# Performance work log

Measured on AMD Instinct MI355X. Metric: run time of the kernel, lower is better.

## Reference

```python
import jax, jax.numpy as jnp
import numpy as np
import math

B, L, D, H = 2, 2048, 1024, 16

def setup_inputs() -> dict:
    key = jax.random.key(0)
    ks = jax.random.split(key, 5)
    return {
        "query": jax.random.normal(ks[0], (B, L, D), dtype=jnp.float32),
        "key": jax.random.normal(ks[1], (B, L, D), dtype=jnp.float32),
        "value": jax.random.normal(ks[2], (B, L, D), dtype=jnp.float32),
        "w_out": jax.random.normal(ks[3], (D, D), dtype=jnp.float32) * (1.0 / math.sqrt(D)),
        "b_out": jnp.zeros((D,), dtype=jnp.float32),
    }

def reference(query, key, value, w_out, b_out):
    b, l, d_model = query.shape
    num_heads = H
    head_dim = d_model // num_heads
    scaling = 1.0 / math.sqrt(d_model)  # NOTE: module scales by embed_dim, not head_dim

    def reshape(x):
        return x.reshape(b, l, num_heads, head_dim).transpose(0, 2, 1, 3)  # [B,H,L,hd]

    q, k, v = reshape(query), reshape(key), reshape(value)
    scores = jnp.einsum("bhqd,bhkd->bhqk", q, k) * scaling  # [B,H,L,L]

    u = max(1, int(math.ceil(math.log(l + 1))))  # static: 8 for L=2048
    _, topk_idx = jax.lax.top_k(scores, u)  # [B,H,L,u]

    # scatter True at top-u key positions per query
    bi = jnp.arange(b)[:, None, None, None]
    hi = jnp.arange(num_heads)[None, :, None, None]
    qi = jnp.arange(l)[None, None, :, None]
    mask = jnp.zeros(scores.shape, dtype=bool).at[bi, hi, qi, topk_idx].set(True)

    scores_masked = jnp.where(mask, scores, -jnp.inf)
    attn_weights = jax.nn.softmax(scores_masked, axis=-1)  # [B,H,L,L]

    attn_out = jnp.einsum("bhqk,bhkd->bhqd", attn_weights, v)
    attn_out = attn_out.transpose(0, 2, 1, 3).reshape(b, l, d_model)
    attn_out = attn_out @ w_out.T + b_out  # nn.Linear
    return attn_out, attn_weights
```

## Files before the change

### kernel.cpp

```cpp
#include <hip/hip_runtime.h>
#include <math.h>

#define BB 2
#define LL 2048
#define DD 1024
#define HH 16
#define SCALE 0.03125f

#define ATTN_ELEMS ((size_t)BB * LL * DD)

typedef unsigned short u16;
typedef __attribute__((ext_vector_type(8))) short bf16x8;
typedef __attribute__((ext_vector_type(4))) short s16x4;
typedef __attribute__((ext_vector_type(4))) float f32x4;

__device__ __forceinline__ u16 f2bf_rne(float f) {
    union { float f; unsigned u; } c; c.f = f;
    unsigned u = c.u;
    u += 0x7fffu + ((u >> 16) & 1u);
    return (u16)(u >> 16);
}

__device__ __forceinline__ void splitbf(float x, short& h, short& l) {
    union { float f; unsigned u; } c; c.f = x;
    unsigned uh = c.u & 0xFFFF0000u;
    h = (short)(uh >> 16);
    union { unsigned u; float f; } ch; ch.u = uh;
    l = (short)f2bf_rne(x - ch.f);
}

__device__ __forceinline__ void insert8(float (&tv)[8], int (&ti)[8], float cv, int ci) {
    bool g0 = cv > tv[0], g1 = cv > tv[1], g2 = cv > tv[2], g3 = cv > tv[3],
         g4 = cv > tv[4], g5 = cv > tv[5], g6 = cv > tv[6];
    tv[7] = g6 ? tv[6] : cv;                 ti[7] = g6 ? ti[6] : ci;
    tv[6] = g5 ? tv[5] : (g6 ? cv : tv[6]);  ti[6] = g5 ? ti[5] : (g6 ? ci : ti[6]);
    tv[5] = g4 ? tv[4] : (g5 ? cv : tv[5]);  ti[5] = g4 ? ti[4] : (g5 ? ci : ti[5]);
    tv[4] = g3 ? tv[3] : (g4 ? cv : tv[4]);  ti[4] = g3 ? ti[3] : (g4 ? ci : ti[4]);
    tv[3] = g2 ? tv[2] : (g3 ? cv : tv[3]);  ti[3] = g2 ? ti[2] : (g3 ? ci : ti[3]);
    tv[2] = g1 ? tv[1] : (g2 ? cv : tv[2]);  ti[2] = g1 ? ti[1] : (g2 ? ci : ti[2]);
    tv[1] = g0 ? tv[0] : (g1 ? cv : tv[1]);  ti[1] = g0 ? ti[0] : (g1 ? ci : ti[1]);
    tv[0] = g0 ? cv : tv[0];                 ti[0] = g0 ? ci : ti[0];
}

__device__ __forceinline__ void insert8t(float (&tv)[8], int (&ti)[8], float cv, int ci) {
    bool g0 = cv > tv[0] || (cv == tv[0] && ci < ti[0]);
    bool g1 = cv > tv[1] || (cv == tv[1] && ci < ti[1]);
    bool g2 = cv > tv[2] || (cv == tv[2] && ci < ti[2]);
    bool g3 = cv > tv[3] || (cv == tv[3] && ci < ti[3]);
    bool g4 = cv > tv[4] || (cv == tv[4] && ci < ti[4]);
    bool g5 = cv > tv[5] || (cv == tv[5] && ci < ti[5]);
    bool g6 = cv > tv[6] || (cv == tv[6] && ci < ti[6]);
    tv[7] = g6 ? tv[6] : cv;                 ti[7] = g6 ? ti[6] : ci;
    tv[6] = g5 ? tv[5] : (g6 ? cv : tv[6]);  ti[6] = g5 ? ti[5] : (g6 ? ci : ti[6]);
    tv[5] = g4 ? tv[4] : (g5 ? cv : tv[5]);  ti[5] = g4 ? ti[4] : (g5 ? ci : ti[5]);
    tv[4] = g3 ? tv[3] : (g4 ? cv : tv[4]);  ti[4] = g3 ? ti[3] : (g4 ? ci : ti[4]);
    tv[3] = g2 ? tv[2] : (g3 ? cv : tv[3]);  ti[3] = g2 ? ti[2] : (g3 ? ci : ti[3]);
    tv[2] = g1 ? tv[1] : (g2 ? cv : tv[2]);  ti[2] = g1 ? ti[1] : (g2 ? ci : ti[2]);
    tv[1] = g0 ? tv[0] : (g1 ? cv : tv[1]);  ti[1] = g0 ? ti[0] : (g1 ? ci : ti[1]);
    tv[0] = g0 ? cv : tv[0];                 ti[0] = g0 ? ci : ti[0];
}

__device__ __forceinline__ void insert12(float (&tv)[12], int (&ti)[12], float cv, int ci) {
    bool g0 = cv > tv[0], g1 = cv > tv[1], g2 = cv > tv[2], g3 = cv > tv[3],
         g4 = cv > tv[4], g5 = cv > tv[5], g6 = cv > tv[6], g7 = cv > tv[7],
         g8 = cv > tv[8], g9 = cv > tv[9], g10 = cv > tv[10];
    tv[11] = g10 ? tv[10] : cv;                 ti[11] = g10 ? ti[10] : ci;
    tv[10] = g9 ? tv[9] : (g10 ? cv : tv[10]);  ti[10] = g9 ? ti[9] : (g10 ? ci : ti[10]);
    tv[9]  = g8 ? tv[8] : (g9 ? cv : tv[9]);    ti[9]  = g8 ? ti[8] : (g9 ? ci : ti[9]);
    tv[8]  = g7 ? tv[7] : (g8 ? cv : tv[8]);    ti[8]  = g7 ? ti[7] : (g8 ? ci : ti[8]);
    tv[7]  = g6 ? tv[6] : (g7 ? cv : tv[7]);    ti[7]  = g6 ? ti[6] : (g7 ? ci : ti[7]);
    tv[6]  = g5 ? tv[5] : (g6 ? cv : tv[6]);    ti[6]  = g5 ? ti[5] : (g6 ? ci : ti[6]);
    tv[5]  = g4 ? tv[4] : (g5 ? cv : tv[5]);    ti[5]  = g4 ? ti[4] : (g5 ? ci : ti[5]);
    tv[4]  = g3 ? tv[3] : (g4 ? cv : tv[4]);    ti[4]  = g3 ? ti[3] : (g4 ? ci : ti[4]);
    tv[3]  = g2 ? tv[2] : (g3 ? cv : tv[3]);    ti[3]  = g2 ? ti[2] : (g3 ? ci : ti[3]);
    tv[2]  = g1 ? tv[1] : (g2 ? cv : tv[2]);    ti[2]  = g1 ? ti[1] : (g2 ? ci : ti[2]);
    tv[1]  = g0 ? tv[0] : (g1 ? cv : tv[1]);    ti[1]  = g0 ? ti[0] : (g1 ? ci : ti[1]);
    tv[0]  = g0 ? cv : tv[0];                   ti[0]  = g0 ? ci : ti[0];
}

__device__ __forceinline__ void merge4(
    const float* v0, const int* i0, const float* v1, const int* i1,
    const float* v2, const int* i2, const float* v3, const int* i3,
    float* ov, int* oi)
{
    int p0 = 0, p1 = 0, p2 = 0, p3 = 0;
    #pragma unroll
    for (int s = 0; s < 8; ++s) {
        float a0 = v0[p0], a1 = v1[p1], a2 = v2[p2], a3 = v3[p3];
        int   b0 = i0[p0], b1 = i1[p1], b2 = i2[p2], b3 = i3[p3];
        float bv = a0; int bi = b0; int bc = 0;
        if (a1 > bv || (a1 == bv && b1 < bi)) { bv = a1; bi = b1; bc = 1; }
        if (a2 > bv || (a2 == bv && b2 < bi)) { bv = a2; bi = b2; bc = 2; }
        if (a3 > bv || (a3 == bv && b3 < bi)) { bv = a3; bi = b3; bc = 3; }
        p0 += (bc == 0); p1 += (bc == 1); p2 += (bc == 2); p3 += (bc == 3);
        ov[s] = bv; oi[s] = bi;
    }
}


__global__ __launch_bounds__(256) void prep_k_kernel(
    const float* __restrict__ k, u16* __restrict__ khi, u16* __restrict__ klo)
{
    int gid = blockIdx.x * 256 + threadIdx.x;
    int li   = gid & 15;
    int qd   = (gid >> 4) & 3;
    int c    = (gid >> 6) & 1;
    int s    = (gid >> 7) & 127;
    int head = gid >> 14;
    int b = head >> 4, h = head & 15;
    const float* src = k + ((size_t)(b * LL + s * 16 + li)) * DD + h * 64 + c * 32 + qd * 8;
    float x[8];
    *(f32x4*)x       = *(const f32x4*)src;
    *(f32x4*)(x + 4) = *(const f32x4*)(src + 4);
    bf16x8 h8, l8;
    #pragma unroll
    for (int e = 0; e < 8; ++e) { short hh, ll; splitbf(x[e], hh, ll); h8[e] = hh; l8[e] = ll; }
    *(bf16x8*)&khi[(size_t)gid * 8] = h8;
    *(bf16x8*)&klo[(size_t)gid * 8] = l8;
}

__global__ __launch_bounds__(256) void prep_w_kernel(
    const float* __restrict__ w, u16* __restrict__ whi, u16* __restrict__ wlo)
{
    int gid = blockIdx.x * 256 + threadIdx.x;
    int li = gid & 15;
    int qd = (gid >> 4) & 3;
    int c  = (gid >> 6) & 3;
    int nt = (gid >> 8) & 3;
    int kc = (gid >> 10) & 7;
    int nb = gid >> 13;
    const float* src = w + (size_t)(nb * 64 + nt * 16 + li) * DD + kc * 128 + c * 32 + qd * 8;
    float x[8];
    *(f32x4*)x       = *(const f32x4*)src;
    *(f32x4*)(x + 4) = *(const f32x4*)(src + 4);
    bf16x8 h8, l8;
    #pragma unroll
    for (int e = 0; e < 8; ++e) { short hh, ll; splitbf(x[e], hh, ll); h8[e] = hh; l8[e] = ll; }
    *(bf16x8*)&whi[(size_t)gid * 8] = h8;
    *(bf16x8*)&wlo[(size_t)gid * 8] = l8;
}

__global__ __launch_bounds__(256) void attn_fast_kernel(
    const float* __restrict__ q, const float* __restrict__ k, const float* __restrict__ v,
    const u16* __restrict__ khi_g, const u16* __restrict__ klo_g,
    float* __restrict__ aw, u16* __restrict__ chi, u16* __restrict__ clo)
{
    const int swz  = (blockIdx.x & 7) * 128 + (blockIdx.x >> 3);
    const int qt   = swz & 31;
    const int h    = (swz >> 5) & 15;
    const int b    = swz >> 9;
    const int t    = threadIdx.x;
    const int wv   = t >> 6;
    const int lane = t & 63;
    const int li   = lane & 15;
    const int quad = lane >> 4;

    __shared__ __align__(16) char arena[19968];
    u16*   gsel = (u16*)(arena);
    float* dv   = (float*)(arena + 1536);
    u16*   dg   = (u16*)(arena + 13824);
    float* s2v  = (float*)(arena + 1536);
    u16*   s2i  = (u16*)(arena + 9728);
    float* wrow = (float*)(arena + 13824);
    u16*   wixs = (u16*)(arena + 15872);

    f32x4* awz = (f32x4*)(aw + (((size_t)(b * HH + h) * LL) + (size_t)qt * 64) * LL);
    const f32x4 zero4 = {0.f, 0.f, 0.f, 0.f};

    bf16x8 qh0, ql0, qh1, ql1;
    {
        const float* qrow = q + ((size_t)(b * LL + qt * 64 + wv * 16 + li)) * DD + h * 64;
        float x[8];
        *(f32x4*)x       = *(const f32x4*)(qrow + quad * 8);
        *(f32x4*)(x + 4) = *(const f32x4*)(qrow + quad * 8 + 4);
        #pragma unroll
        for (int e = 0; e < 8; ++e) { short hh, ll; splitbf(x[e], hh, ll); qh0[e] = hh; ql0[e] = ll; }
        *(f32x4*)x       = *(const f32x4*)(qrow + 32 + quad * 8);
        *(f32x4*)(x + 4) = *(const f32x4*)(qrow + 32 + quad * 8 + 4);
        #pragma unroll
        for (int e = 0; e < 8; ++e) { short hh, ll; splitbf(x[e], hh, ll); qh1[e] = hh; ql1[e] = ll; }
    }

    float tv[12]; int tg[12];
    #pragma unroll
    for (int s = 0; s < 12; ++s) { tv[s] = -INFINITY; tg[s] = 0; }

    const u16* khb = khi_g + (size_t)(b * HH + h) * 131072 + (size_t)lane * 8;
    const u16* klb = klo_g + (size_t)(b * HH + h) * 131072 + (size_t)lane * 8;

    bf16x8 Ah0 = *(const bf16x8*)(khb);
    bf16x8 Ah1 = *(const bf16x8*)(khb + 512);
    bf16x8 Al0 = *(const bf16x8*)(klb);
    bf16x8 Al1 = *(const bf16x8*)(klb + 512);
    bf16x8 Bh0 = *(const bf16x8*)(khb + 1024);
    bf16x8 Bh1 = *(const bf16x8*)(khb + 1536);
    bf16x8 Bl0 = *(const bf16x8*)(klb + 1024);
    bf16x8 Bl1 = *(const bf16x8*)(klb + 1536);

    for (int sp = 0; sp < 64; ++sp) {
        const int spn = (sp + 1) & 63;
        const size_t off = (size_t)spn * 2048;
        bf16x8 NAh0 = *(const bf16x8*)(khb + off);
        bf16x8 NAh1 = *(const bf16x8*)(khb + off + 512);
        bf16x8 NAl0 = *(const bf16x8*)(klb + off);
        bf16x8 NAl1 = *(const bf16x8*)(klb + off + 512);
        bf16x8 NBh0 = *(const bf16x8*)(khb + off + 1024);
        bf16x8 NBh1 = *(const bf16x8*)(khb + off + 1536);
        bf16x8 NBl0 = *(const bf16x8*)(klb + off + 1024);
        bf16x8 NBl1 = *(const bf16x8*)(klb + off + 1536);

        awz[sp * 512 + t]       = zero4;
        awz[sp * 512 + 256 + t] = zero4;

        f32x4 c4a = {0,0,0,0}, c4b = {0,0,0,0}, d4a = {0,0,0,0}, d4b = {0,0,0,0};
        c4a = __builtin_amdgcn_mfma_f32_16x16x32_bf16(Ah0, qh0, c4a, 0, 0, 0);
        c4b = __builtin_amdgcn_mfma_f32_16x16x32_bf16(Ah1, qh1, c4b, 0, 0, 0);
        d4a = __builtin_amdgcn_mfma_f32_16x16x32_bf16(Bh0, qh0, d4a, 0, 0, 0);
        d4b = __builtin_amdgcn_mfma_f32_16x16x32_bf16(Bh1, qh1, d4b, 0, 0, 0);
        c4a = __builtin_amdgcn_mfma_f32_16x16x32_bf16(Al0, qh0, c4a, 0, 0, 0);
        c4b = __builtin_amdgcn_mfma_f32_16x16x32_bf16(Al1, qh1, c4b, 0, 0, 0);
        d4a = __builtin_amdgcn_mfma_f32_16x16x32_bf16(Bl0, qh0, d4a, 0, 0, 0);
        d4b = __builtin_amdgcn_mfma_f32_16x16x32_bf16(Bl1, qh1, d4b, 0, 0, 0);
        c4a = __builtin_amdgcn_mfma_f32_16x16x32_bf16(Ah0, ql0, c4a, 0, 0, 0);
        c4b = __builtin_amdgcn_mfma_f32_16x16x32_bf16(Ah1, ql1, c4b, 0, 0, 0);
        d4a = __builtin_amdgcn_mfma_f32_16x16x32_bf16(Bh0, ql0, d4a, 0, 0, 0);
        d4b = __builtin_amdgcn_mfma_f32_16x16x32_bf16(Bh1, ql1, d4b, 0, 0, 0);

        float s0 = c4a[0] + c4b[0], s1 = c4a[1] + c4b[1];
        float s2 = c4a[2] + c4b[2], s3 = c4a[3] + c4b[3];
        float s4 = d4a[0] + d4b[0], s5 = d4a[1] + d4b[1];
        float s6 = d4a[2] + d4b[2], s7 = d4a[3] + d4b[3];
        float m = fmaxf(fmaxf(fmaxf(s0, s1), fmaxf(s2, s3)),
                        fmaxf(fmaxf(s4, s5), fmaxf(s6, s7)));
        if (m > tv[11]) insert12(tv, tg, m, sp * 32 + quad * 4);

        Ah0 = NAh0; Ah1 = NAh1; Al0 = NAl0; Al1 = NAl1;
        Bh0 = NBh0; Bh1 = NBh1; Bl0 = NBl0; Bl1 = NBl1;
    }

    {
        const int row = wv * 16 + li;
        #pragma unroll
        for (int s = 0; s < 12; ++s) {
            dv[row * 48 + quad * 12 + s] = tv[s];
            dg[row * 48 + quad * 12 + s] = (u16)tg[s];
        }
    }
    __syncthreads();

    if (t < 64) {
        const float* v0 = &dv[t * 48];       const u16* i0 = &dg[t * 48];
        const float* v1 = &dv[t * 48 + 12];  const u16* i1 = &dg[t * 48 + 12];
        const float* v2 = &dv[t * 48 + 24];  const u16* i2 = &dg[t * 48 + 24];
        const float* v3 = &dv[t * 48 + 36];  const u16* i3 = &dg[t * 48 + 36];
        int p0 = 0, p1 = 0, p2 = 0, p3 = 0;
        #pragma unroll
        for (int s = 0; s < 12; ++s) {
            float a0 = v0[p0], a1 = v1[p1], a2 = v2[p2], a3 = v3[p3];
            int   b0 = i0[p0], b1 = i1[p1], b2 = i2[p2], b3 = i3[p3];
            float bv = a0; int bi = b0; int bc = 0;
            if (a1 > bv || (a1 == bv && b1 < bi)) { bv = a1; bi = b1; bc = 1; }
            if (a2 > bv || (a2 == bv && b2 < bi)) { bv = a2; bi = b2; bc = 2; }
            if (a3 > bv || (a3 == bv && b3 < bi)) { bv = a3; bi = b3; bc = 3; }
            p0 += (bc == 0); p1 += (bc == 1); p2 += (bc == 2); p3 += (bc == 3);
            gsel[t * 12 + s] = (u16)bi;
        }
    }
    __syncthreads();

    {
        const int row = t >> 2, p = t & 3;
        const float* qp = q + ((size_t)(b * LL + qt * 64 + row)) * DD + h * 64;
        float tv8[8]; int ti8[8];
        #pragma unroll
        for (int s = 0; s < 8; ++s) { tv8[s] = -INFINITY; ti8[s] = 0x7fffffff; }
        for (int j = p * 24; j < p * 24 + 24; ++j) {
            int gk = (int)gsel[row * 12 + (j >> 3)];
            int e  = j & 7;
            int kidx = gk + ((e >> 2) << 4) + (e & 3);
            const float* kp = k + ((size_t)(b * LL + kidx)) * DD + h * 64;
            float a0 = 0.f, a1 = 0.f, a2 = 0.f, a3 = 0.f;
            for (int d4 = 0; d4 < 16; ++d4) {
                f32x4 qa = *(const f32x4*)(qp + d4 * 4);
                f32x4 ka = *(const f32x4*)(kp + d4 * 4);
                a0 = fmaf(qa[0], ka[0], a0);
                a1 = fmaf(qa[1], ka[1], a1);
                a2 = fmaf(qa[2], ka[2], a2);
                a3 = fmaf(qa[3], ka[3], a3);
            }
            float sc = ((a0 + a1) + (a2 + a3)) * SCALE;
            if (sc > tv8[7] || (sc == tv8[7] && kidx < ti8[7])) insert8t(tv8, ti8, sc, kidx);
        }
        #pragma unroll
        for (int s = 0; s < 8; ++s) {
            s2v[(row * 4 + p) * 8 + s] = tv8[s];
            s2i[(row * 4 + p) * 8 + s] = (u16)ti8[s];
        }
    }
    __syncthreads();

    if (t < 64) {
        const float* v0 = &s2v[(t * 4 + 0) * 8]; const u16* i0 = &s2i[(t * 4 + 0) * 8];
        const float* v1 = &s2v[(t * 4 + 1) * 8]; const u16* i1 = &s2i[(t * 4 + 1) * 8];
        const float* v2 = &s2v[(t * 4 + 2) * 8]; const u16* i2 = &s2i[(t * 4 + 2) * 8];
        const float* v3 = &s2v[(t * 4 + 3) * 8]; const u16* i3 = &s2i[(t * 4 + 3) * 8];
        int p0 = 0, p1 = 0, p2 = 0, p3 = 0;
        float fv[8]; int fi[8];
        #pragma unroll
        for (int s = 0; s < 8; ++s) {
            float a0 = v0[p0], a1 = v1[p1], a2 = v2[p2], a3 = v3[p3];
            int   b0 = i0[p0], b1 = i1[p1], b2 = i2[p2], b3 = i3[p3];
            float bv = a0; int bi = b0; int bc = 0;
            if (a1 > bv || (a1 == bv && b1 < bi)) { bv = a1; bi = b1; bc = 1; }
            if (a2 > bv || (a2 == bv && b2 < bi)) { bv = a2; bi = b2; bc = 2; }
            if (a3 > bv || (a3 == bv && b3 < bi)) { bv = a3; bi = b3; bc = 3; }
            p0 += (bc == 0); p1 += (bc == 1); p2 += (bc == 2); p3 += (bc == 3);
            fv[s] = bv; fi[s] = bi;
        }
        float m = fv[0];
        float e0[8]; float sum = 0.f;
        #pragma unroll
        for (int s = 0; s < 8; ++s) { e0[s] = __expf(fv[s] - m); sum += e0[s]; }
        float inv = 1.0f / sum;
        float* awrow = aw + (((size_t)(b * HH + h) * LL) + (size_t)qt * 64 + t) * LL;
        #pragma unroll
        for (int s = 0; s < 8; ++s) {
            float w8 = e0[s] * inv;
            awrow[fi[s]] = w8;
            wrow[t * 8 + s] = w8; wixs[t * 8 + s] = (u16)fi[s];
        }
    }
    __syncthreads();

    const float* vbase = v + ((size_t)b * LL) * DD + h * 64;
    #pragma unroll
    for (int i = 0; i < 4; ++i) {
        int id = i * 256 + t;
        int row = id >> 4, seg = id & 15;
        f32x4 acc = {0.f, 0.f, 0.f, 0.f};
        #pragma unroll
        for (int s = 0; s < 8; ++s) {
            float ws = wrow[row * 8 + s];
            f32x4 vvv = *(const f32x4*)(vbase + (size_t)wixs[row * 8 + s] * DD + seg * 4);
            acc[0] = fmaf(ws, vvv[0], acc[0]);
            acc[1] = fmaf(ws, vvv[1], acc[1]);
            acc[2] = fmaf(ws, vvv[2], acc[2]);
            acc[3] = fmaf(ws, vvv[3], acc[3]);
        }
        size_t off = ((size_t)(b * LL + qt * 64 + row)) * DD + h * 64 + seg * 4;
        s16x4 h4, l4;
        #pragma unroll
        for (int j = 0; j < 4; ++j) { short hh, ll; splitbf(acc[j], hh, ll); h4[j] = hh; l4[j] = ll; }
        *(s16x4*)(chi + off) = h4;
        *(s16x4*)(clo + off) = l4;
    }
}

__global__ __launch_bounds__(256) void linear_fast_kernel(
    const u16* __restrict__ chi, const u16* __restrict__ clo,
    const u16* __restrict__ whi, const u16* __restrict__ wlo,
    const float* __restrict__ bias, float* __restrict__ out)
{
    const int bid  = blockIdx.x;
    const int nb   = bid & 15, mb = bid >> 4;
    const int t    = threadIdx.x;
    const int wv   = t >> 6;
    const int lane = t & 63;
    const int li   = lane & 15;
    const int quad = lane >> 4;

    f32x4 acc0 = {0.f,0.f,0.f,0.f}, acc1 = {0.f,0.f,0.f,0.f},
          acc2 = {0.f,0.f,0.f,0.f}, acc3 = {0.f,0.f,0.f,0.f};

    const u16* ah_row = chi + (size_t)(mb * 64 + wv * 16 + li) * DD + quad * 8;
    const u16* al_row = clo + (size_t)(mb * 64 + wv * 16 + li) * DD + quad * 8;
    const size_t wboff = (size_t)nb * 65536 + (size_t)lane * 8;

    for (int kc = 0; kc < 8; ++kc) {
        const u16* wb_h = whi + wboff + kc * 8192;
        const u16* wb_l = wlo + wboff + kc * 8192;
        #pragma unroll
        for (int c = 0; c < 4; ++c) {
            bf16x8 ah = *(const bf16x8*)(ah_row + kc * 128 + c * 32);
            bf16x8 al = *(const bf16x8*)(al_row + kc * 128 + c * 32);
            bf16x8 bh0 = *(const bf16x8*)(wb_h + c * 512);
            bf16x8 bl0 = *(const bf16x8*)(wb_l + c * 512);
            bf16x8 bh1 = *(const bf16x8*)(wb_h + 2048 + c * 512);
            bf16x8 bl1 = *(const bf16x8*)(wb_l + 2048 + c * 512);
            bf16x8 bh2 = *(const bf16x8*)(wb_h + 4096 + c * 512);
            bf16x8 bl2 = *(const bf16x8*)(wb_l + 4096 + c * 512);
            bf16x8 bh3 = *(const bf16x8*)(wb_h + 6144 + c * 512);
            bf16x8 bl3 = *(const bf16x8*)(wb_l + 6144 + c * 512);
            acc0 = __builtin_amdgcn_mfma_f32_16x16x32_bf16(ah, bh0, acc0, 0, 0, 0);
            acc0 = __builtin_amdgcn_mfma_f32_16x16x32_bf16(ah, bl0, acc0, 0, 0, 0);
            acc0 = __builtin_amdgcn_mfma_f32_16x16x32_bf16(al, bh0, acc0, 0, 0, 0);
            acc1 = __builtin_amdgcn_mfma_f32_16x16x32_bf16(ah, bh1, acc1, 0, 0, 0);
            acc1 = __builtin_amdgcn_mfma_f32_16x16x32_bf16(ah, bl1, acc1, 0, 0, 0);
            acc1 = __builtin_amdgcn_mfma_f32_16x16x32_bf16(al, bh1, acc1, 0, 0, 0);
            acc2 = __builtin_amdgcn_mfma_f32_16x16x32_bf16(ah, bh2, acc2, 0, 0, 0);
            acc2 = __builtin_amdgcn_mfma_f32_16x16x32_bf16(ah, bl2, acc2, 0, 0, 0);
            acc2 = __builtin_amdgcn_mfma_f32_16x16x32_bf16(al, bh2, acc2, 0, 0, 0);
            acc3 = __builtin_amdgcn_mfma_f32_16x16x32_bf16(ah, bh3, acc3, 0, 0, 0);
            acc3 = __builtin_amdgcn_mfma_f32_16x16x32_bf16(ah, bl3, acc3, 0, 0, 0);
            acc3 = __builtin_amdgcn_mfma_f32_16x16x32_bf16(al, bh3, acc3, 0, 0, 0);
        }
    }

    #pragma unroll
    for (int st = 0; st < 4; ++st) {
        f32x4 a = (st == 0) ? acc0 : (st == 1) ? acc1 : (st == 2) ? acc2 : acc3;
        int col = nb * 64 + st * 16 + li;
        float bb2 = bias[col];
        #pragma unroll
        for (int r = 0; r < 4; ++r)
            out[(size_t)(mb * 64 + wv * 16 + quad * 4 + r) * DD + col] = a[r] + bb2;
    }
}


__global__ __launch_bounds__(256) void attn_kernel(
    const float* __restrict__ q, const float* __restrict__ k, const float* __restrict__ v,
    float* __restrict__ aw, float* __restrict__ ctx)
{
    const int bid  = blockIdx.x;
    const int qt   = bid & 31;
    const int h    = (bid >> 5) & 15;
    const int b    = bid >> 9;
    const int t    = threadIdx.x;
    const int wv   = t >> 6;
    const int lane = t & 63;
    const int li   = lane & 15;
    const int quad = lane >> 4;

    __shared__ __align__(16) char smA[32768];
    __shared__ float s2v[32][4][8];
    __shared__ int   s2i[32][4][8];
    __shared__ int   cidx[32][12];
    __shared__ float cs[32][12];
    __shared__ float wrow[64][8];
    __shared__ int   wix[64][8];
    u16* khi = (u16*)smA;
    u16* klo = (u16*)(smA + 16384);

    const float* kbase = k + ((size_t)b * LL) * DD + h * 64;
    f32x4* awz = (f32x4*)(aw + (((size_t)(b * HH + h) * LL) + (size_t)qt * 64) * LL);
    const f32x4 zero4 = {0.f, 0.f, 0.f, 0.f};

    bf16x8 qh0, ql0, qh1, ql1;
    {
        const float* qrow = q + ((size_t)(b * LL + qt * 64 + wv * 16 + li)) * DD + h * 64;
        float x[8];
        *(f32x4*)x       = *(const f32x4*)(qrow + quad * 8);
        *(f32x4*)(x + 4) = *(const f32x4*)(qrow + quad * 8 + 4);
        #pragma unroll
        for (int e = 0; e < 8; ++e) { short hh, ll; splitbf(x[e], hh, ll); qh0[e] = hh; ql0[e] = ll; }
        *(f32x4*)x       = *(const f32x4*)(qrow + 32 + quad * 8);
        *(f32x4*)(x + 4) = *(const f32x4*)(qrow + 32 + quad * 8 + 4);
        #pragma unroll
        for (int e = 0; e < 8; ++e) { short hh, ll; splitbf(x[e], hh, ll); qh1[e] = hh; ql1[e] = ll; }
    }

    float tv[4][8]; int tix[4][8];
    #pragma unroll
    for (int r = 0; r < 4; ++r)
        #pragma unroll
        for (int s = 0; s < 8; ++s) { tv[r][s] = -INFINITY; tix[r][s] = 0; }

    for (int iter = 0; iter < 16; ++iter) {
        __syncthreads();
        #pragma unroll
        for (int j = 0; j < 4; ++j) {
            int f   = j * 256 + t;
            int col = f >> 3;
            int c   = (f >> 2) & 1;
            int qd  = f & 3;
            const float* src = kbase + (size_t)(iter * 128 + col) * DD + c * 32 + qd * 8;
            float x[8];
            *(f32x4*)x       = *(const f32x4*)src;
            *(f32x4*)(x + 4) = *(const f32x4*)(src + 4);
            bf16x8 h8, l8;
            #pragma unroll
            for (int e = 0; e < 8; ++e) { short hh, ll; splitbf(x[e], hh, ll); h8[e] = hh; l8[e] = ll; }
            int off = (((col >> 4) * 2 + c) << 9) + (qd << 7) + ((col & 15) << 3);
            *(bf16x8*)&khi[off] = h8;
            *(bf16x8*)&klo[off] = l8;
        }
        #pragma unroll
        for (int i = 0; i < 8; ++i) awz[iter * 2048 + i * 256 + t] = zero4;
        __syncthreads();

        #pragma unroll
        for (int s = 0; s < 8; ++s) {
            int fo = s << 10;
            bf16x8 kh0 = *(bf16x8*)&khi[fo + (lane << 3)];
            bf16x8 kh1 = *(bf16x8*)&khi[fo + 512 + (lane << 3)];
            bf16x8 kl0 = *(bf16x8*)&klo[fo + (lane << 3)];
            bf16x8 kl1 = *(bf16x8*)&klo[fo + 512 + (lane << 3)];
            f32x4 c4 = {0.f, 0.f, 0.f, 0.f};
            c4 = __builtin_amdgcn_mfma_f32_16x16x32_bf16(qh0, kh0, c4, 0, 0, 0);
            c4 = __builtin_amdgcn_mfma_f32_16x16x32_bf16(qh1, kh1, c4, 0, 0, 0);
            c4 = __builtin_amdgcn_mfma_f32_16x16x32_bf16(qh0, kl0, c4, 0, 0, 0);
            c4 = __builtin_amdgcn_mfma_f32_16x16x32_bf16(qh1, kl1, c4, 0, 0, 0);
            c4 = __builtin_amdgcn_mfma_f32_16x16x32_bf16(ql0, kh0, c4, 0, 0, 0);
            c4 = __builtin_amdgcn_mfma_f32_16x16x32_bf16(ql1, kh1, c4, 0, 0, 0);
            int ci = iter * 128 + s * 16 + li;
            #pragma unroll
            for (int r = 0; r < 4; ++r) {
                float cv = c4[r] * SCALE;
                if (cv > tv[r][7]) insert8(tv[r], tix[r], cv, ci);
            }
        }
    }

    float* mv = (float*)smA;
    int*   mi = (int*)(smA + 16384);
    for (int bb = 0; bb < 2; ++bb) {
        __syncthreads();
        if ((wv >> 1) == bb) {
            int rl0 = (wv & 1) * 16 + quad * 4;
            #pragma unroll
            for (int r = 0; r < 4; ++r) {
                int base = (rl0 + r) * 128 + li * 8;
                #pragma unroll
                for (int s = 0; s < 8; ++s) { mv[base + s] = tv[r][s]; mi[base + s] = tix[r][s]; }
            }
        }
        __syncthreads();
        if (t < 128) {
            int rr = t >> 2, p = t & 3;
            int base = rr * 128 + p * 32;
            merge4(&mv[base], &mi[base], &mv[base + 8], &mi[base + 8],
                   &mv[base + 16], &mi[base + 16], &mv[base + 24], &mi[base + 24],
                   s2v[rr][p], s2i[rr][p]);
        }
        __syncthreads();
        if (t < 32) {
            int rr = t;
            int pp[4] = {0, 0, 0, 0};
            #pragma unroll
            for (int s = 0; s < 12; ++s) {
                float bv = -INFINITY; int bi = 0x7fffffff; int bc = 0;
                #pragma unroll
                for (int l = 0; l < 4; ++l) {
                    if (pp[l] < 8) {
                        float hv = s2v[rr][l][pp[l]]; int hi2 = s2i[rr][l][pp[l]];
                        if (hv > bv || (hv == bv && hi2 < bi)) { bv = hv; bi = hi2; bc = l; }
                    }
                }
                pp[bc] += 1;
                cidx[rr][s] = bi;
            }
        }
        __syncthreads();
        for (int task = t; task < 384; task += 256) {
            int row = task / 12, c = task - row * 12;
            const float* qp = q + ((size_t)(b * LL + qt * 64 + bb * 32 + row)) * DD + h * 64;
            const float* kp = k + ((size_t)(b * LL + cidx[row][c])) * DD + h * 64;
            float acc = 0.f;
            for (int d4 = 0; d4 < 16; ++d4) {
                f32x4 qa = *(const f32x4*)(qp + d4 * 4);
                f32x4 ka = *(const f32x4*)(kp + d4 * 4);
                acc = fmaf(qa[0], ka[0], acc);
                acc = fmaf(qa[1], ka[1], acc);
                acc = fmaf(qa[2], ka[2], acc);
                acc = fmaf(qa[3], ka[3], acc);
            }
            cs[row][c] = acc * SCALE;
        }
        __syncthreads();
        if (t < 32) {
            int rr = t;
            float vv[12]; int ii[12];
            #pragma unroll
            for (int c = 0; c < 12; ++c) { vv[c] = cs[rr][c]; ii[c] = cidx[rr][c]; }
            float fv[8]; int fi[8];
            #pragma unroll
            for (int s = 0; s < 8; ++s) {
                float bv = -INFINITY; int bi = 0x7fffffff; int bc = 0;
                #pragma unroll
                for (int c = 0; c < 12; ++c) {
                    if (vv[c] > bv || (vv[c] == bv && ii[c] < bi)) { bv = vv[c]; bi = ii[c]; bc = c; }
                }
                vv[bc] = -INFINITY;
                fv[s] = bv; fi[s] = bi;
            }
            float m = fv[0];
            float e0[8]; float sum = 0.f;
            #pragma unroll
            for (int s = 0; s < 8; ++s) { e0[s] = __expf(fv[s] - m); sum += e0[s]; }
            float inv = 1.0f / sum;
            int grow = bb * 32 + rr;
            float* awrow = aw + (((size_t)(b * HH + h) * LL) + (size_t)qt * 64 + grow) * LL;
            #pragma unroll
            for (int s = 0; s < 8; ++s) {
                float w8 = e0[s] * inv;
                awrow[fi[s]] = w8;
                wrow[grow][s] = w8; wix[grow][s] = fi[s];
            }
        }
    }
    __syncthreads();

    const float* vbase = v + ((size_t)b * LL) * DD + h * 64;
    #pragma unroll
    for (int i = 0; i < 4; ++i) {
        int id = i * 256 + t;
        int row = id >> 4, seg = id & 15;
        f32x4 acc = {0.f, 0.f, 0.f, 0.f};
        #pragma unroll
        for (int s = 0; s < 8; ++s) {
            float ws = wrow[row][s];
            f32x4 vvv = *(const f32x4*)(vbase + (size_t)wix[row][s] * DD + seg * 4);
            acc[0] = fmaf(ws, vvv[0], acc[0]);
            acc[1] = fmaf(ws, vvv[1], acc[1]);
            acc[2] = fmaf(ws, vvv[2], acc[2]);
            acc[3] = fmaf(ws, vvv[3], acc[3]);
        }
        *(f32x4*)(ctx + ((size_t)(b * LL + qt * 64 + row)) * DD + h * 64 + seg * 4) = acc;
    }
}

__global__ __launch_bounds__(256) void linear_ws_kernel(
    const float* __restrict__ ctx, const float* __restrict__ w,
    const float* __restrict__ bias, float* __restrict__ out)
{
    const int bid  = blockIdx.x;
    const int nb   = bid & 15, mb = bid >> 4;
    const int t    = threadIdx.x;
    const int wv   = t >> 6;
    const int lane = t & 63;
    const int li   = lane & 15;
    const int quad = lane >> 4;

    __shared__ u16 bhi[8192], blo[8192];

    f32x4 acc0 = {0.f,0.f,0.f,0.f}, acc1 = {0.f,0.f,0.f,0.f},
          acc2 = {0.f,0.f,0.f,0.f}, acc3 = {0.f,0.f,0.f,0.f};
    const float* arow = ctx + (size_t)(mb * 64 + wv * 16 + li) * DD;

    for (int kc = 0; kc < 8; ++kc) {
        __syncthreads();
        #pragma unroll
        for (int j = 0; j < 4; ++j) {
            int f   = j * 256 + t;
            int col = f >> 4;
            int c   = (f >> 2) & 3;
            int qd  = f & 3;
            const float* src = w + (size_t)(nb * 64 + col) * DD + kc * 128 + c * 32 + qd * 8;
            float x[8];
            *(f32x4*)x       = *(const f32x4*)src;
            *(f32x4*)(x + 4) = *(const f32x4*)(src + 4);
            bf16x8 h8, l8;
            #pragma unroll
            for (int e = 0; e < 8; ++e) { short hh, ll; splitbf(x[e], hh, ll); h8[e] = hh; l8[e] = ll; }
            int off = (((col >> 4) * 4 + c) << 9) + (qd << 7) + ((col & 15) << 3);
            *(bf16x8*)&bhi[off] = h8;
            *(bf16x8*)&blo[off] = l8;
        }
        __syncthreads();

        bf16x8 ah[4], al[4];
        #pragma unroll
        for (int c = 0; c < 4; ++c) {
            float x[8];
            *(f32x4*)x       = *(const f32x4*)(arow + kc * 128 + c * 32 + quad * 8);
            *(f32x4*)(x + 4) = *(const f32x4*)(arow + kc * 128 + c * 32 + quad * 8 + 4);
            #pragma unroll
            for (int e = 0; e < 8; ++e) { short hh, ll; splitbf(x[e], hh, ll); ah[c][e] = hh; al[c][e] = ll; }
        }
        #pragma unroll
        for (int c = 0; c < 4; ++c) {
            bf16x8 bh0 = *(bf16x8*)&bhi[(( 0 + c) << 9) + (lane << 3)];
            bf16x8 bl0 = *(bf16x8*)&blo[(( 0 + c) << 9) + (lane << 3)];
            bf16x8 bh1 = *(bf16x8*)&bhi[(( 4 + c) << 9) + (lane << 3)];
            bf16x8 bl1 = *(bf16x8*)&blo[(( 4 + c) << 9) + (lane << 3)];
            bf16x8 bh2 = *(bf16x8*)&bhi[(( 8 + c) << 9) + (lane << 3)];
            bf16x8 bl2 = *(bf16x8*)&blo[(( 8 + c) << 9) + (lane << 3)];
            bf16x8 bh3 = *(bf16x8*)&bhi[((12 + c) << 9) + (lane << 3)];
            bf16x8 bl3 = *(bf16x8*)&blo[((12 + c) << 9) + (lane << 3)];
            acc0 = __builtin_amdgcn_mfma_f32_16x16x32_bf16(ah[c], bh0, acc0, 0, 0, 0);
            acc0 = __builtin_amdgcn_mfma_f32_16x16x32_bf16(ah[c], bl0, acc0, 0, 0, 0);
            acc0 = __builtin_amdgcn_mfma_f32_16x16x32_bf16(al[c], bh0, acc0, 0, 0, 0);
            acc1 = __builtin_amdgcn_mfma_f32_16x16x32_bf16(ah[c], bh1, acc1, 0, 0, 0);
            acc1 = __builtin_amdgcn_mfma_f32_16x16x32_bf16(ah[c], bl1, acc1, 0, 0, 0);
            acc1 = __builtin_amdgcn_mfma_f32_16x16x32_bf16(al[c], bh1, acc1, 0, 0, 0);
            acc2 = __builtin_amdgcn_mfma_f32_16x16x32_bf16(ah[c], bh2, acc2, 0, 0, 0);
            acc2 = __builtin_amdgcn_mfma_f32_16x16x32_bf16(ah[c], bl2, acc2, 0, 0, 0);
            acc2 = __builtin_amdgcn_mfma_f32_16x16x32_bf16(al[c], bh2, acc2, 0, 0, 0);
            acc3 = __builtin_amdgcn_mfma_f32_16x16x32_bf16(ah[c], bh3, acc3, 0, 0, 0);
            acc3 = __builtin_amdgcn_mfma_f32_16x16x32_bf16(ah[c], bl3, acc3, 0, 0, 0);
            acc3 = __builtin_amdgcn_mfma_f32_16x16x32_bf16(al[c], bh3, acc3, 0, 0, 0);
        }
    }

    #pragma unroll
    for (int st = 0; st < 4; ++st) {
        f32x4 a = (st == 0) ? acc0 : (st == 1) ? acc1 : (st == 2) ? acc2 : acc3;
        int col = nb * 64 + st * 16 + li;
        float bb2 = bias[col];
        #pragma unroll
        for (int r = 0; r < 4; ++r)
            out[(size_t)(mb * 64 + wv * 16 + quad * 4 + r) * DD + col] = a[r] + bb2;
    }
}

__global__ __launch_bounds__(256) void linear_inplace_kernel(
    float* io, const float* __restrict__ w, const float* __restrict__ bias)
{
    __shared__ u16 ahi[16384], alo[16384];
    const int t    = threadIdx.x;
    const int m0   = blockIdx.x * 16;
    const int wv   = t >> 6;
    const int lane = t & 63;
    const int li   = lane & 15;
    const int quad = lane >> 4;

    #pragma unroll
    for (int i = 0; i < 8; ++i) {
        int id  = i * 256 + t;
        int row = id >> 7;
        int c   = (id >> 2) & 31;
        int qd  = id & 3;
        const float* src = io + (size_t)(m0 + row) * DD + c * 32 + qd * 8;
        float x[8];
        *(f32x4*)x       = *(const f32x4*)src;
        *(f32x4*)(x + 4) = *(const f32x4*)(src + 4);
        bf16x8 h8, l8;
        #pragma unroll
        for (int e = 0; e < 8; ++e) { short hh, ll; splitbf(x[e], hh, ll); h8[e] = hh; l8[e] = ll; }
        int off = (c << 9) + (qd << 7) + (row << 3);
        *(bf16x8*)&ahi[off] = h8;
        *(bf16x8*)&alo[off] = l8;
    }
    __syncthreads();

    f32x4 acc[16];
    #pragma unroll
    for (int i = 0; i < 16; ++i) acc[i] = (f32x4){0.f, 0.f, 0.f, 0.f};

    for (int c = 0; c < 32; ++c) {
        bf16x8 ah = *(bf16x8*)&ahi[(c << 9) + (lane << 3)];
        bf16x8 al = *(bf16x8*)&alo[(c << 9) + (lane << 3)];
        #pragma unroll
        for (int sub = 0; sub < 16; ++sub) {
            int col = wv * 256 + sub * 16 + li;
            const float* src = w + (size_t)col * DD + c * 32 + quad * 8;
            float x[8];
            *(f32x4*)x       = *(const f32x4*)src;
            *(f32x4*)(x + 4) = *(const f32x4*)(src + 4);
            bf16x8 bh, bl;
            #pragma unroll
            for (int e = 0; e < 8; ++e) { short hh, ll; splitbf(x[e], hh, ll); bh[e] = hh; bl[e] = ll; }
            acc[sub] = __builtin_amdgcn_mfma_f32_16x16x32_bf16(ah, bh, acc[sub], 0, 0, 0);
            acc[sub] = __builtin_amdgcn_mfma_f32_16x16x32_bf16(ah, bl, acc[sub], 0, 0, 0);
            acc[sub] = __builtin_amdgcn_mfma_f32_16x16x32_bf16(al, bh, acc[sub], 0, 0, 0);
        }
    }

    #pragma unroll
    for (int sub = 0; sub < 16; ++sub) {
        int col = wv * 256 + sub * 16 + li;
        float bb2 = bias[col];
        #pragma unroll
        for (int r = 0; r < 4; ++r)
            io[(size_t)(m0 + quad * 4 + r) * DD + col] = acc[sub][r] + bb2;
    }
}

extern "C" void kernel_launch(void* const* d_in, const int* in_sizes, int n_in,
                              void* d_out, int out_size, void* d_ws, size_t ws_size,
                              hipStream_t stream) {
    const float* q    = (const float*)d_in[0];
    const float* k    = (const float*)d_in[1];
    const float* v    = (const float*)d_in[2];
    const float* w    = (const float*)d_in[3];
    const float* bias = (const float*)d_in[4];

    float* out = (float*)d_out;
    float* aw  = out + ATTN_ELEMS;

    const size_t CHI_ELE = ATTN_ELEMS;
    const size_t KSP_ELE = 4194304;
    const size_t WSP_ELE = 1048576;
    const size_t need_fast = (2 * CHI_ELE + 2 * KSP_ELE + 2 * WSP_ELE) * sizeof(u16);

    if (d_ws != nullptr && ws_size >= need_fast) {
        u16* chi = (u16*)d_ws;
        u16* clo = chi + CHI_ELE;
        u16* khi = clo + CHI_ELE;
        u16* klo = khi + KSP_ELE;
        u16* whi = klo + KSP_ELE;
        u16* wlo = whi + WSP_ELE;
        prep_k_kernel<<<2048, 256, 0, stream>>>(k, khi, klo);
        prep_w_kernel<<<512, 256, 0, stream>>>(w, whi, wlo);
        attn_fast_kernel<<<BB * HH * (LL / 64), 256, 0, stream>>>(q, k, v, khi, klo, aw, chi, clo);
        linear_fast_kernel<<<(BB * LL / 64) * (DD / 64), 256, 0, stream>>>(chi, clo, whi, wlo, bias, out);
    } else {
        const bool use_ws = (d_ws != nullptr) && (ws_size >= ATTN_ELEMS * sizeof(float));
        float* ctx = use_ws ? (float*)d_ws : out;
        attn_kernel<<<BB * HH * (LL / 64), 256, 0, stream>>>(q, k, v, aw, ctx);
        if (use_ws) {
            linear_ws_kernel<<<(BB * LL / 64) * (DD / 64), 256, 0, stream>>>(ctx, w, bias, out);
        } else {
            linear_inplace_kernel<<<BB * LL / 16, 256, 0, stream>>>(out, w, bias);
        }
    }
}
```

Baseline: 935.1 us.

## Tune attn kernel: occupancy hint, unroll, register-cached q, padded LDS staging

```diff
diff --git a/kernel.cpp b/kernel.cpp
--- a/kernel.cpp
+++ b/kernel.cpp
@@ -140,7 +140,7 @@
     *(bf16x8*)&wlo[(size_t)gid * 8] = l8;
 }
 
-__global__ __launch_bounds__(256) void attn_fast_kernel(
+__global__ __launch_bounds__(256, 4) void attn_fast_kernel(
     const float* __restrict__ q, const float* __restrict__ k, const float* __restrict__ v,
     const u16* __restrict__ khi_g, const u16* __restrict__ klo_g,
     float* __restrict__ aw, u16* __restrict__ chi, u16* __restrict__ clo)
@@ -155,14 +155,14 @@
     const int li   = lane & 15;
     const int quad = lane >> 4;
 
-    __shared__ __align__(16) char arena[19968];
+    __shared__ __align__(16) char arena[21504];
     u16*   gsel = (u16*)(arena);
     float* dv   = (float*)(arena + 1536);
     u16*   dg   = (u16*)(arena + 13824);
     float* s2v  = (float*)(arena + 1536);
-    u16*   s2i  = (u16*)(arena + 9728);
-    float* wrow = (float*)(arena + 13824);
-    u16*   wixs = (u16*)(arena + 15872);
+    u16*   s2i  = (u16*)(arena + 13824);
+    float* wrow = (float*)(arena + 18432);
+    u16*   wixs = (u16*)(arena + 20480);
 
     f32x4* awz = (f32x4*)(aw + (((size_t)(b * HH + h) * LL) + (size_t)qt * 64) * LL);
     const f32x4 zero4 = {0.f, 0.f, 0.f, 0.f};
@@ -197,6 +197,7 @@
     bf16x8 Bl0 = *(const bf16x8*)(klb + 1024);
     bf16x8 Bl1 = *(const bf16x8*)(klb + 1536);
 
+    #pragma unroll 2
     for (int sp = 0; sp < 64; ++sp) {
         const int spn = (sp + 1) & 63;
         const size_t off = (size_t)spn * 2048;
@@ -271,39 +272,52 @@
     {
         const int row = t >> 2, p = t & 3;
         const float* qp = q + ((size_t)(b * LL + qt * 64 + row)) * DD + h * 64;
+        f32x4 qr[16];
+        #pragma unroll
+        for (int d4 = 0; d4 < 16; ++d4) qr[d4] = *(const f32x4*)(qp + d4 * 4);
         float tv8[8]; int ti8[8];
         #pragma unroll
         for (int s = 0; s < 8; ++s) { tv8[s] = -INFINITY; ti8[s] = 0x7fffffff; }
-        for (int j = p * 24; j < p * 24 + 24; ++j) {
-            int gk = (int)gsel[row * 12 + (j >> 3)];
-            int e  = j & 7;
-            int kidx = gk + ((e >> 2) << 4) + (e & 3);
-            const float* kp = k + ((size_t)(b * LL + kidx)) * DD + h * 64;
+        for (int jj = 0; jj < 24; jj += 2) {
+            int gk = (int)gsel[row * 12 + p * 3 + (jj >> 3)];
+            int e  = jj & 7;
+            int k0 = gk + ((e >> 2) << 4) + (e & 3);
+            int k1 = k0 + 1;
+            const float* kp0 = k + ((size_t)(b * LL + k0)) * DD + h * 64;
+            const float* kp1 = k + ((size_t)(b * LL + k1)) * DD + h * 64;
             float a0 = 0.f, a1 = 0.f, a2 = 0.f, a3 = 0.f;
+            float b0 = 0.f, b1 = 0.f, b2 = 0.f, b3 = 0.f;
+            #pragma unroll
             for (int d4 = 0; d4 < 16; ++d4) {
-                f32x4 qa = *(const f32x4*)(qp + d4 * 4);
-                f32x4 ka = *(const f32x4*)(kp + d4 * 4);
-                a0 = fmaf(qa[0], ka[0], a0);
-                a1 = fmaf(qa[1], ka[1], a1);
-                a2 = fmaf(qa[2], ka[2], a2);
-                a3 = fmaf(qa[3], ka[3], a3);
+                f32x4 ka = *(const f32x4*)(kp0 + d4 * 4);
+                f32x4 kb = *(const f32x4*)(kp1 + d4 * 4);
+                a0 = fmaf(qr[d4][0], ka[0], a0);
+                a1 = fmaf(qr[d4][1], ka[1], a1);
+                a2 = fmaf(qr[d4][2], ka[2], a2);
+                a3 = fmaf(qr[d4][3], ka[3], a3);
+                b0 = fmaf(qr[d4][0], kb[0], b0);
+                b1 = fmaf(qr[d4][1], kb[1], b1);
+                b2 = fmaf(qr[d4][2], kb[2], b2);
+                b3 = fmaf(qr[d4][3], kb[3], b3);
             }
-            float sc = ((a0 + a1) + (a2 + a3)) * SCALE;
-            if (sc > tv8[7] || (sc == tv8[7] && kidx < ti8[7])) insert8t(tv8, ti8, sc, kidx);
+            float sc0 = ((a0 + a1) + (a2 + a3)) * SCALE;
+            float sc1 = ((b0 + b1) + (b2 + b3)) * SCALE;
+            if (sc0 > tv8[7] || (sc0 == tv8[7] && k0 < ti8[7])) insert8t(tv8, ti8, sc0, k0);
+            if (sc1 > tv8[7] || (sc1 == tv8[7] && k1 < ti8[7])) insert8t(tv8, ti8, sc1, k1);
         }
         #pragma unroll
         for (int s = 0; s < 8; ++s) {
-            s2v[(row * 4 + p) * 8 + s] = tv8[s];
-            s2i[(row * 4 + p) * 8 + s] = (u16)ti8[s];
+            s2v[(row * 4 + p) * 9 + s] = tv8[s];
+            s2i[(row * 4 + p) * 9 + s] = (u16)ti8[s];
         }
     }
     __syncthreads();
 
     if (t < 64) {
-        const float* v0 = &s2v[(t * 4 + 0) * 8]; const u16* i0 = &s2i[(t * 4 + 0) * 8];
-        const float* v1 = &s2v[(t * 4 + 1) * 8]; const u16* i1 = &s2i[(t * 4 + 1) * 8];
-        const float* v2 = &s2v[(t * 4 + 2) * 8]; const u16* i2 = &s2i[(t * 4 + 2) * 8];
-        const float* v3 = &s2v[(t * 4 + 3) * 8]; const u16* i3 = &s2i[(t * 4 + 3) * 8];
+        const float* v0 = &s2v[(t * 4 + 0) * 9]; const u16* i0 = &s2i[(t * 4 + 0) * 9];
+        const float* v1 = &s2v[(t * 4 + 1) * 9]; const u16* i1 = &s2i[(t * 4 + 1) * 9];
+        const float* v2 = &s2v[(t * 4 + 2) * 9]; const u16* i2 = &s2i[(t * 4 + 2) * 9];
+        const float* v3 = &s2v[(t * 4 + 3) * 9]; const u16* i3 = &s2i[(t * 4 + 3) * 9];
         int p0 = 0, p1 = 0, p2 = 0, p3 = 0;
         float fv[8]; int fi[8];
         #pragma unroll
```

Result: slower. 1.093 ms (+16.9%).
